# Kernel tuning notes

Hardware: AMD Instinct MI355X
Metric: run time of the kernel (lower is better)

## Reference

```python
import jax, jax.numpy as jnp
import numpy as np

DIM = 768
H = 12          # num_heads
HD = DIM // H   # head_dim = 64
WS = 128        # window_size
SHIFT = 64      # shift_size
NPATCH = 128    # num_patches for relative bias
MLP = 3072
EPS = 1e-5


def _layernorm(x, w, b):
    m = jnp.mean(x, axis=-1, keepdims=True)
    v = jnp.mean(jnp.square(x - m), axis=-1, keepdims=True)
    return (x - m) * jax.lax.rsqrt(v + EPS) * w + b


def _window_attention(xw, mw, qkv_w, qkv_b, proj_w, proj_b, rel_bias):
    # xw: [Bw, ws, C] windows, mw: [Bw, ws] bool valid-key mask
    Bw, N, C = xw.shape
    qkv = (xw @ qkv_w + qkv_b).reshape(Bw, N, 3, H, HD)
    qkv = jnp.transpose(qkv, (2, 0, 3, 1, 4))  # [3, Bw, H, N, hd]
    q, k, v = qkv[0], qkv[1], qkv[2]
    attn = jnp.einsum('bhqd,bhkd->bhqk', q, k) * (HD ** -0.5)
    # relative position bias: table [2*NPATCH-1, H] gathered by index [N, N]
    coords = jnp.arange(N)
    rel_idx = coords[None, :] - coords[:, None] + (NPATCH - 1)  # [N, N]
    bias = jnp.transpose(rel_bias[rel_idx], (2, 0, 1))  # [H, N, N]
    attn = attn + bias[None]
    neg = jnp.finfo(attn.dtype).min
    attn = jnp.where(mw[:, None, None, :], attn, neg)  # mask invalid keys
    attn = jax.nn.softmax(attn, axis=-1)
    attn = jnp.nan_to_num(attn, nan=0.0)
    out = jnp.einsum('bhqk,bhkd->bqhd', attn, v).reshape(Bw, N, C)
    return out @ proj_w + proj_b


def reference(x, norm1_w, norm1_b, qkv_w, qkv_b, proj_w, proj_b, rel_bias,
              ls1, norm2_w, norm2_b, fc1_w, fc1_b, fc2_w, fc2_b, ls2):
    B, N, C = x.shape
    # ---- attention branch: norm1 -> shifted-window attention ----
    h = _layernorm(x, norm1_w, norm1_b)
    pad = (-N) % WS
    hp = jnp.pad(h, ((0, 0), (0, pad), (0, 0)))  # zero-pad sequence
    Npad = N + pad
    valid = jnp.broadcast_to(jnp.arange(Npad) < N, (B, Npad))
    if SHIFT > 0:
        hp = jnp.roll(hp, -SHIFT, axis=1)
        valid = jnp.roll(valid, -SHIFT, axis=1)
    nw = Npad // WS
    xw = hp.reshape(B * nw, WS, C)
    mw = valid.reshape(B * nw, WS)
    aw = _window_attention(xw, mw, qkv_w, qkv_b, proj_w, proj_b, rel_bias)
    a = aw.reshape(B, Npad, C)
    if SHIFT > 0:
        a = jnp.roll(a, SHIFT, axis=1)
    a = a[:, :N, :]
    x = x + a * ls1  # LayerScale, DropPath is identity
    # ---- MLP branch ----
    h2 = _layernorm(x, norm2_w, norm2_b)
    m = jax.nn.gelu(h2 @ fc1_w + fc1_b, approximate=False) @ fc2_w + fc2_b
    return x + m * ls2


def setup_inputs() -> dict:
    key = jax.random.key(0)
    ks = jax.random.split(key, 8)
    B, N = 16, 2000
    s = 0.02
    return {
        'x': jax.random.normal(ks[0], (B, N, DIM), jnp.float32),
        'norm1_w': jnp.ones((DIM,), jnp.float32),
        'norm1_b': jnp.zeros((DIM,), jnp.float32),
        'qkv_w': s * jax.random.normal(ks[1], (DIM, 3 * DIM), jnp.float32),
        'qkv_b': jnp.zeros((3 * DIM,), jnp.float32),
        'proj_w': s * jax.random.normal(ks[2], (DIM, DIM), jnp.float32),
        'proj_b': jnp.zeros((DIM,), jnp.float32),
        'rel_bias': s * jax.random.normal(ks[3], (2 * NPATCH - 1, H), jnp.float32),
        'ls1': 1e-5 * jnp.ones((DIM,), jnp.float32),
        'norm2_w': jnp.ones((DIM,), jnp.float32),
        'norm2_b': jnp.zeros((DIM,), jnp.float32),
        'fc1_w': s * jax.random.normal(ks[4], (DIM, MLP), jnp.float32),
        'fc1_b': jnp.zeros((MLP,), jnp.float32),
        'fc2_w': s * jax.random.normal(ks[5], (MLP, DIM), jnp.float32),
        'fc2_b': jnp.zeros((DIM,), jnp.float32),
        'ls2': 1e-5 * jnp.ones((DIM,), jnp.float32),
    }
```

## Files before the change

kernel.cpp:

```cpp
#include <hip/hip_runtime.h>
#include <hip/hip_bf16.h>

typedef unsigned short u16;
typedef unsigned char u8;
typedef __attribute__((ext_vector_type(8))) short bh8;
typedef __attribute__((ext_vector_type(4))) float fx4;
typedef __attribute__((ext_vector_type(4))) int i32x4;
typedef __attribute__((ext_vector_type(8))) int i32x8;

__device__ __forceinline__ u16 f2bf(float f) {
  union { float f; unsigned u; } v; v.f = f;
  unsigned r = v.u + 0x7FFFu + ((v.u >> 16) & 1u);
  return (u16)(r >> 16);
}

__device__ __forceinline__ u8 f2fp8(float x) {
  union { float f; unsigned u; } v; v.f = x;
  const unsigned sign = (v.u >> 24) & 0x80u;
  v.u &= 0x7FFFFFFFu;
  if (v.f >= 464.0f) return (u8)(sign | 0x7Eu);
  if (v.f < 0.015625f) {
    int q = (int)rintf(v.f * 512.0f);
    return (u8)(sign | (unsigned)q);
  }
  unsigned u2 = v.u + 0x7FFFFu + ((v.u >> 20) & 1u);
  unsigned e2 = (u2 >> 23) - 127u + 7u;
  unsigned mant = (u2 >> 20) & 7u;
  return (u8)(sign | (e2 << 3) | mant);
}

__device__ __forceinline__ void cvt2_fp8(float a, float b, u8& x, u8& y) {
#if __has_builtin(__builtin_amdgcn_cvt_pk_fp8_f32)
  int r = __builtin_amdgcn_cvt_pk_fp8_f32(a, b, 0, false);
  x = (u8)(r & 0xff);
  y = (u8)((r >> 8) & 0xff);
#else
  x = f2fp8(a);
  y = f2fp8(b);
#endif
}

__device__ __forceinline__ float fp8_manual(u8 b) {
  unsigned s = b >> 7, e = (b >> 3) & 15, m = b & 7;
  float v;
  if (e == 0) {
    v = m * 0.001953125f;
  } else {
    union { unsigned u; float f; } t;
    t.u = ((e + 120u) << 23) | (m << 20);
    v = t.f;
  }
  return s ? -v : v;
}

__device__ __forceinline__ void fp8dec4(unsigned w, float* o) {
#if __has_builtin(__builtin_amdgcn_cvt_f32_fp8)
  o[0] = __builtin_amdgcn_cvt_f32_fp8((int)w, 0);
  o[1] = __builtin_amdgcn_cvt_f32_fp8((int)w, 1);
  o[2] = __builtin_amdgcn_cvt_f32_fp8((int)w, 2);
  o[3] = __builtin_amdgcn_cvt_f32_fp8((int)w, 3);
#else
  o[0] = fp8_manual((u8)(w & 0xffu));
  o[1] = fp8_manual((u8)((w >> 8) & 0xffu));
  o[2] = fp8_manual((u8)((w >> 16) & 0xffu));
  o[3] = fp8_manual((u8)((w >> 24) & 0xffu));
#endif
}

__device__ __forceinline__ void gload_lds16(const void* g, void* l) {
  __builtin_amdgcn_global_load_lds(
      (const __attribute__((address_space(1))) void*)g,
      (__attribute__((address_space(3))) void*)l, 16, 0, 0);
}

__device__ __forceinline__ i32x8 rd32(const char* p0, const char* p1) {
  i32x4 lo = *(const i32x4*)p0;
  i32x4 hi = *(const i32x4*)p1;
  return __builtin_shufflevector(lo, hi, 0, 1, 2, 3, 4, 5, 6, 7);
}

__global__ __launch_bounds__(256) void transp_cvt(
    const float* __restrict__ W, u8* __restrict__ Wt, int K, int N) {
  __shared__ float tile[32][33];
  const int k0 = blockIdx.x * 32, n0 = blockIdx.y * 32;
  const int tx = threadIdx.x & 31, ty = threadIdx.x >> 5;
#pragma unroll
  for (int i = 0; i < 4; ++i)
    tile[ty + i * 8][tx] = W[(size_t)(k0 + ty + i * 8) * N + n0 + tx];
  __syncthreads();
#pragma unroll
  for (int i = 0; i < 4; ++i)
    Wt[(size_t)(n0 + ty + i * 8) * K + k0 + tx] = f2fp8(tile[tx][ty + i * 8] * 32.0f);
}

__device__ __forceinline__ float blockSum(float v, float* sh) {
#pragma unroll
  for (int m = 32; m; m >>= 1) v += __shfl_xor(v, m);
  if ((threadIdx.x & 63) == 0) sh[threadIdx.x >> 6] = v;
  __syncthreads();
  return sh[0] + sh[1] + sh[2] + sh[3];
}

__global__ __launch_bounds__(256) void ln1_k(
    const float* __restrict__ x, const float* __restrict__ w,
    const float* __restrict__ b, u8* __restrict__ hw) {
  __shared__ float sh1[4], sh2[4];
  const int row = blockIdx.x;
  const int bI = row >> 11, i = row & 2047;
  const int j = (i + 64) & 2047;
  const int tid = threadIdx.x;
  u8* dst = hw + (size_t)row * 768;
  if (j >= 2000) {
    dst[tid] = 0; dst[tid + 256] = 0; dst[tid + 512] = 0;
    return;
  }
  const float* xr = x + ((size_t)bI * 2000 + j) * 768;
  float v0 = xr[tid], v1 = xr[tid + 256], v2 = xr[tid + 512];
  float mean = blockSum(v0 + v1 + v2, sh1) * (1.0f / 768.0f);
  float d0 = v0 - mean, d1 = v1 - mean, d2 = v2 - mean;
  float var = blockSum(d0 * d0 + d1 * d1 + d2 * d2, sh2) * (1.0f / 768.0f);
  float rs = rsqrtf(var + 1e-5f);
  u8 x0, x1, x2, xd;
  cvt2_fp8((d0 * rs * w[tid] + b[tid]) * 4.0f,
           (d1 * rs * w[tid + 256] + b[tid + 256]) * 4.0f, x0, x1);
  cvt2_fp8((d2 * rs * w[tid + 512] + b[tid + 512]) * 4.0f, 0.0f, x2, xd);
  dst[tid] = x0; dst[tid + 256] = x1; dst[tid + 512] = x2;
}

__global__ __launch_bounds__(256) void ln2_k(
    const float* __restrict__ src, const float* __restrict__ w,
    const float* __restrict__ b, u8* __restrict__ dsth) {
  __shared__ float sh1[4], sh2[4];
  const int row = blockIdx.x;
  const int tid = threadIdx.x;
  const float* xr = src + (size_t)row * 768;
  u8* dst = dsth + (size_t)row * 768;
  float v0 = xr[tid], v1 = xr[tid + 256], v2 = xr[tid + 512];
  float mean = blockSum(v0 + v1 + v2, sh1) * (1.0f / 768.0f);
  float d0 = v0 - mean, d1 = v1 - mean, d2 = v2 - mean;
  float var = blockSum(d0 * d0 + d1 * d1 + d2 * d2, sh2) * (1.0f / 768.0f);
  float rs = rsqrtf(var + 1e-5f);
  u8 x0, x1, x2, xd;
  cvt2_fp8((d0 * rs * w[tid] + b[tid]) * 4.0f,
           (d1 * rs * w[tid + 256] + b[tid + 256]) * 4.0f, x0, x1);
  cvt2_fp8((d2 * rs * w[tid + 512] + b[tid + 512]) * 4.0f, 0.0f, x2, xd);
  dst[tid] = x0; dst[tid + 256] = x1; dst[tid + 512] = x2;
}

enum { EQKV = 0, EPROJ = 1, EFC1 = 2, EFC2 = 3 };

template <int EPI>
__global__ __launch_bounds__(256, 3) void gemm128f8(
    const u8* __restrict__ A, const u8* __restrict__ Bt,
    const float* __restrict__ bias, const float* __restrict__ lsv,
    const float* __restrict__ resid, float* __restrict__ outf,
    u8* __restrict__ outb,
    int gn, int N, int K, int mValid) {
  __shared__ u8 LDSBUF[32768];
  u8* As = LDSBUF;
  u8* Bs = LDSBUF + 16384;
  const int tid = threadIdx.x;
  const int lane = tid & 63, wid = tid >> 6;
  const int wr = wid >> 1, wc = wid & 1;

  const int nwg = gridDim.x, bid = blockIdx.x;
  const int q = nwg >> 3, r = nwg & 7;
  const int xcd = bid & 7, idx = bid >> 3;
  const int wg = (xcd < r ? xcd * (q + 1) : r * (q + 1) + (xcd - r) * q) + idx;
  const int mt = wg / gn, nt = wg % gn;
  const int m0 = mt * 128, n0 = nt * 128;
  const int NT = K >> 7;

  fx4 acc[4][4];
#pragma unroll
  for (int i = 0; i < 4; ++i)
#pragma unroll
    for (int j = 0; j < 4; ++j) acc[i][j] = fx4{0.f, 0.f, 0.f, 0.f};

  const int rsel = lane & 15, kgrp = lane >> 4;
  const int colb = kgrp * 32;
  const int xorc = (rsel & 7) << 4;

  const int rl = tid >> 3;
  const int kc16 = ((tid & 7) ^ (rl & 7)) * 16;
  const u8* aRow = A + (size_t)(m0 + rl) * K + kc16;
  const u8* bRow = Bt + (size_t)(n0 + rl) * K + kc16;

  for (int t = 0; t < NT; ++t) {
    const int k0 = t << 7;
#pragma unroll
    for (int i = 0; i < 4; ++i) {
      gload_lds16(aRow + (size_t)k0 + (size_t)(i * 32) * K,
                  (char*)As + i * 4096 + wid * 1024);
      gload_lds16(bRow + (size_t)k0 + (size_t)(i * 32) * K,
                  (char*)Bs + i * 4096 + wid * 1024);
    }
    __syncthreads();
    i32x8 af[4];
#pragma unroll
    for (int mi = 0; mi < 4; ++mi) {
      const char* ab = (const char*)As + (wr * 64 + mi * 16 + rsel) * 128;
      af[mi] = rd32(ab + (colb ^ xorc), ab + ((colb + 16) ^ xorc));
    }
#pragma unroll
    for (int ni = 0; ni < 4; ++ni) {
      const char* bb = (const char*)Bs + (wc * 64 + ni * 16 + rsel) * 128;
      i32x8 bfr = rd32(bb + (colb ^ xorc), bb + ((colb + 16) ^ xorc));
#pragma unroll
      for (int mi = 0; mi < 4; ++mi)
        acc[mi][ni] = __builtin_amdgcn_mfma_scale_f32_16x16x128_f8f6f4(
            af[mi], bfr, acc[mi][ni], 0, 0, 0, 125, 0, 122);
    }
    __syncthreads();
  }

  const int cc = lane & 15;
  const int rq = (lane >> 4) * 4;

  if (EPI == EQKV || EPI == EFC1) {
    u8* Ls = LDSBUF;
#pragma unroll
    for (int ni = 0; ni < 4; ++ni) {
      const int col = wc * 64 + ni * 16 + cc;
      const float bv = bias[n0 + col];
#pragma unroll
      for (int mi = 0; mi < 4; ++mi) {
#pragma unroll
        for (int jp = 0; jp < 2; ++jp) {
          float va = acc[mi][ni][jp * 2] + bv;
          float vb = acc[mi][ni][jp * 2 + 1] + bv;
          if (EPI == EFC1) {
            va = va / (1.0f + __expf(-1.702f * va));
            vb = vb / (1.0f + __expf(-1.702f * vb));
          }
          u8 xa, xb;
          cvt2_fp8(va * 4.0f, vb * 4.0f, xa, xb);
          const int row = wr * 64 + mi * 16 + rq + jp * 2;
          const int s = (row & 12) << 2;
          Ls[row * 128 + (col ^ s)] = xa;
          Ls[(row + 1) * 128 + (col ^ s)] = xb;
        }
      }
    }
    __syncthreads();
#pragma unroll
    for (int i = 0; i < 4; ++i) {
      const int row = i * 32 + (tid >> 3);
      const int s = (row & 12) << 2;
      i32x4 v = *(const i32x4*)(Ls + row * 128 + (((tid & 7) * 16) ^ s));
      *(i32x4*)(outb + (size_t)(m0 + row) * N + n0 + (tid & 7) * 16) = v;
    }
  } else {
    float* Lf = (float*)LDSBUF;
#pragma unroll
    for (int p = 0; p < 2; ++p) {
      if (p) __syncthreads();
      if (wc == p) {
#pragma unroll
        for (int ni = 0; ni < 4; ++ni) {
          const int gc = n0 + p * 64 + ni * 16 + cc;
          const float bv = bias[gc], ls = lsv[gc];
#pragma unroll
          for (int mi = 0; mi < 4; ++mi)
#pragma unroll
            for (int j = 0; j < 4; ++j) {
              const int row = wr * 64 + mi * 16 + rq + j;
              const int s = (row & 12) << 2;
              Lf[row * 64 + ((ni * 16 + cc) ^ s)] = (acc[mi][ni][j] + bv) * ls;
            }
        }
      }
      __syncthreads();
#pragma unroll
      for (int i = 0; i < 8; ++i) {
        const int row = i * 16 + (tid >> 4);
        const int gr = m0 + row;
        const int s = (row & 12) << 2;
        fx4 sv = *(const fx4*)(Lf + row * 64 + (((tid & 15) * 4) ^ s));
        if (EPI == EFC2) {
          if (gr < mValid) {
            float* po = outf + (size_t)gr * 768 + n0 + p * 64 + (tid & 15) * 4;
            fx4 cur = *(const fx4*)po;
            *(fx4*)po = fx4{cur[0] + sv[0], cur[1] + sv[1], cur[2] + sv[2], cur[3] + sv[3]};
          }
        } else {
          const int bI = gr >> 11, ip = gr & 2047;
          const int jj = (ip + 64) & 2047;
          if (jj < 2000) {
            const size_t o = ((size_t)bI * 2000 + jj) * 768 + n0 + p * 64 + (tid & 15) * 4;
            fx4 rv = *(const fx4*)(resid + o);
            *(fx4*)(outf + o) = fx4{rv[0] + sv[0], rv[1] + sv[1], rv[2] + sv[2], rv[3] + sv[3]};
          }
        }
      }
    }
  }
}

struct AttnLds {
  union {
    struct { u16 Qs[128][72]; u16 Ks[128][72]; } qk;
    u16 Ps[128][136];
  } u;
  u16 Vt[64][136];
  float biasv[256];
};

__global__ __launch_bounds__(256, 2) void attn_k(
    const u8* __restrict__ qkv8, const float* __restrict__ rel_bias,
    u8* __restrict__ aout) {
  __shared__ AttnLds L;
  const int blk = blockIdx.x;
  const int w = blk / 12, h = blk - w * 12;
  const int wi = w & 15;
  const int tid = threadIdx.x;
  const int lane = tid & 63, wid = tid >> 6;

  if (tid < 255) L.biasv[tid] = rel_bias[tid * 12 + h];

  const size_t rowbase = (size_t)w * 128;
#pragma unroll
  for (int i = 0; i < 4; ++i) {
    const int idx = tid + i * 256;
    const int r = idx >> 3, seg = idx & 7;
    const u8* src = qkv8 + (rowbase + r) * 2304 + h * 64 + seg * 8;
    unsigned qlo = *(const unsigned*)(src);
    unsigned qhi = *(const unsigned*)(src + 4);
    unsigned klo = *(const unsigned*)(src + 768);
    unsigned khi = *(const unsigned*)(src + 772);
    unsigned vlo = *(const unsigned*)(src + 1536);
    unsigned vhi = *(const unsigned*)(src + 1540);
    float qf[8], kf[8], vf[8];
    fp8dec4(qlo, qf); fp8dec4(qhi, qf + 4);
    fp8dec4(klo, kf); fp8dec4(khi, kf + 4);
    fp8dec4(vlo, vf); fp8dec4(vhi, vf + 4);
    bh8 qv, kv;
    u16 va[8];
#pragma unroll
    for (int e = 0; e < 8; ++e) {
      qv[e] = (short)f2bf(qf[e] * 0.25f);
      kv[e] = (short)f2bf(kf[e] * 0.25f);
      va[e] = f2bf(vf[e] * 0.25f);
    }
    *(bh8*)&L.u.qk.Qs[r][seg * 8] = qv;
    *(bh8*)&L.u.qk.Ks[r][seg * 8] = kv;
#pragma unroll
    for (int e = 0; e < 8; ++e) L.Vt[seg * 8 + e][r] = va[e];
  }
  __syncthreads();

  const int R0 = wid * 32;
  const int rsel = lane & 15, kgrp = lane >> 4;
  fx4 s[2][8];
#pragma unroll
  for (int mi = 0; mi < 2; ++mi)
#pragma unroll
    for (int ni = 0; ni < 8; ++ni) s[mi][ni] = fx4{0.f, 0.f, 0.f, 0.f};

#pragma unroll
  for (int ks = 0; ks < 2; ++ks) {
    bh8 aq[2], bk[8];
#pragma unroll
    for (int mi = 0; mi < 2; ++mi)
      aq[mi] = *(const bh8*)&L.u.qk.Qs[R0 + mi * 16 + rsel][ks * 32 + kgrp * 8];
#pragma unroll
    for (int ni = 0; ni < 8; ++ni)
      bk[ni] = *(const bh8*)&L.u.qk.Ks[ni * 16 + rsel][ks * 32 + kgrp * 8];
#pragma unroll
    for (int mi = 0; mi < 2; ++mi)
#pragma unroll
      for (int ni = 0; ni < 8; ++ni)
        s[mi][ni] = __builtin_amdgcn_mfma_f32_16x16x32_bf16(aq[mi], bk[ni], s[mi][ni], 0, 0, 0);
  }

#pragma unroll
  for (int mi = 0; mi < 2; ++mi) {
#pragma unroll
    for (int j = 0; j < 4; ++j) {
      const int r = R0 + mi * 16 + kgrp * 4 + j;
      float vals[8];
      float mx = -1e30f;
#pragma unroll
      for (int ni = 0; ni < 8; ++ni) {
        const int c = ni * 16 + rsel;
        const int ic = wi * 128 + c;
        const bool valid = ((ic + 64) & 2047) < 2000;
        const float v = valid ? (s[mi][ni][j] * 0.125f + L.biasv[c - r + 127]) : -1e30f;
        vals[ni] = v;
        mx = fmaxf(mx, v);
      }
#pragma unroll
      for (int mm = 8; mm; mm >>= 1) mx = fmaxf(mx, __shfl_xor(mx, mm));
      float sum = 0.f;
#pragma unroll
      for (int ni = 0; ni < 8; ++ni) { float p = __expf(vals[ni] - mx); vals[ni] = p; sum += p; }
#pragma unroll
      for (int mm = 8; mm; mm >>= 1) sum += __shfl_xor(sum, mm);
      const float inv = 1.0f / sum;
#pragma unroll
      for (int ni = 0; ni < 8; ++ni) s[mi][ni][j] = vals[ni] * inv;
    }
  }
  __syncthreads();

#pragma unroll
  for (int mi = 0; mi < 2; ++mi)
#pragma unroll
    for (int ni = 0; ni < 8; ++ni)
#pragma unroll
      for (int j = 0; j < 4; ++j)
        L.u.Ps[R0 + mi * 16 + kgrp * 4 + j][ni * 16 + rsel] = f2bf(s[mi][ni][j]);
  __syncthreads();

  fx4 o[2][4];
#pragma unroll
  for (int mi = 0; mi < 2; ++mi)
#pragma unroll
    for (int ni = 0; ni < 4; ++ni) o[mi][ni] = fx4{0.f, 0.f, 0.f, 0.f};
#pragma unroll
  for (int ks = 0; ks < 4; ++ks) {
    bh8 ap[2], bv[4];
#pragma unroll
    for (int mi = 0; mi < 2; ++mi)
      ap[mi] = *(const bh8*)&L.u.Ps[R0 + mi * 16 + rsel][ks * 32 + kgrp * 8];
#pragma unroll
    for (int ni = 0; ni < 4; ++ni)
      bv[ni] = *(const bh8*)&L.Vt[ni * 16 + rsel][ks * 32 + kgrp * 8];
#pragma unroll
    for (int mi = 0; mi < 2; ++mi)
#pragma unroll
      for (int ni = 0; ni < 4; ++ni)
        o[mi][ni] = __builtin_amdgcn_mfma_f32_16x16x32_bf16(ap[mi], bv[ni], o[mi][ni], 0, 0, 0);
  }

#pragma unroll
  for (int mi = 0; mi < 2; ++mi)
#pragma unroll
    for (int ni = 0; ni < 4; ++ni)
#pragma unroll
      for (int jp = 0; jp < 2; ++jp) {
        u8 xa, xb;
        cvt2_fp8(o[mi][ni][jp * 2] * 4.0f, o[mi][ni][jp * 2 + 1] * 4.0f, xa, xb);
        const size_t r0 = rowbase + R0 + mi * 16 + kgrp * 4 + jp * 2;
        aout[r0 * 768 + h * 64 + ni * 16 + rsel] = xa;
        aout[(r0 + 1) * 768 + h * 64 + ni * 16 + rsel] = xb;
      }
}

extern "C" void kernel_launch(void* const* d_in, const int* in_sizes, int n_in,
                              void* d_out, int out_size, void* d_ws, size_t ws_size,
                              hipStream_t stream) {
  (void)in_sizes; (void)n_in; (void)out_size; (void)ws_size;
  const float* x        = (const float*)d_in[0];
  const float* n1w      = (const float*)d_in[1];
  const float* n1b      = (const float*)d_in[2];
  const float* qkv_w    = (const float*)d_in[3];
  const float* qkv_b    = (const float*)d_in[4];
  const float* proj_w   = (const float*)d_in[5];
  const float* proj_b   = (const float*)d_in[6];
  const float* rel_bias = (const float*)d_in[7];
  const float* ls1      = (const float*)d_in[8];
  const float* n2w      = (const float*)d_in[9];
  const float* n2b      = (const float*)d_in[10];
  const float* fc1_w    = (const float*)d_in[11];
  const float* fc1_b    = (const float*)d_in[12];
  const float* fc2_w    = (const float*)d_in[13];
  const float* fc2_b    = (const float*)d_in[14];
  const float* ls2      = (const float*)d_in[15];
  float* out = (float*)d_out;

  char* ws = (char*)d_ws;
  u8*  WtQ   = (u8*)(ws);
  u8*  WtP   = (u8*)(ws + 3538944);
  u8*  WtF1  = (u8*)(ws + 4718592);
  u8*  WtF2  = (u8*)(ws + 9437184);
  u8*  bufB8 = (u8*)(ws + 14155776);
  u8*  bufA8 = (u8*)(ws + 14155776 + 50331648);

  dim3 t256(256);
  transp_cvt<<<dim3(24, 72), t256, 0, stream>>>(qkv_w, WtQ, 768, 2304);
  transp_cvt<<<dim3(24, 24), t256, 0, stream>>>(proj_w, WtP, 768, 768);
  transp_cvt<<<dim3(24, 96), t256, 0, stream>>>(fc1_w, WtF1, 768, 3072);
  transp_cvt<<<dim3(96, 24), t256, 0, stream>>>(fc2_w, WtF2, 3072, 768);

  ln1_k<<<32768, t256, 0, stream>>>(x, n1w, n1b, bufB8);
  gemm128f8<EQKV><<<dim3(256 * 18), t256, 0, stream>>>(
      bufB8, WtQ, qkv_b, nullptr, nullptr, nullptr, bufA8, 18, 2304, 768, 32768);
  attn_k<<<3072, t256, 0, stream>>>(bufA8, rel_bias, bufB8);
  gemm128f8<EPROJ><<<dim3(256 * 6), t256, 0, stream>>>(
      bufB8, WtP, proj_b, ls1, x, out, nullptr, 6, 768, 768, 32768);
  ln2_k<<<32000, t256, 0, stream>>>(out, n2w, n2b, bufB8);
  gemm128f8<EFC1><<<dim3(250 * 24), t256, 0, stream>>>(
      bufB8, WtF1, fc1_b, nullptr, nullptr, nullptr, bufA8, 24, 3072, 768, 32000);
  gemm128f8<EFC2><<<dim3(250 * 6), t256, 0, stream>>>(
      bufA8, WtF2, fc2_b, ls2, nullptr, out, nullptr, 6, 768, 3072, 32000);
}
```

Before: 502.6 us.

## Use 8 waves per block in FP8 GEMM with 64x32 per-wave tiles

Doubles the GEMM workgroup from 256 to 512 threads. Each wave now computes a 64x32 sub-tile instead of 64x64, so accumulator registers are halved and per-thread global-to-LDS loads drop from 8 to 4. The epilogues are remapped to the new wave layout. The aim is more waves in flight to hide latency, at the cost of more LDS fragment reads per MFMA, since each A fragment is reused only twice.

```diff
diff --git a/kernel.cpp b/kernel.cpp
--- a/kernel.cpp
+++ b/kernel.cpp
@@ -150,7 +150,7 @@
 enum { EQKV = 0, EPROJ = 1, EFC1 = 2, EFC2 = 3 };
 
 template <int EPI>
-__global__ __launch_bounds__(256, 3) void gemm128f8(
+__global__ __launch_bounds__(512, 4) void gemm128f8(
     const u8* __restrict__ A, const u8* __restrict__ Bt,
     const float* __restrict__ bias, const float* __restrict__ lsv,
     const float* __restrict__ resid, float* __restrict__ outf,
@@ -161,7 +161,7 @@
   u8* Bs = LDSBUF + 16384;
   const int tid = threadIdx.x;
   const int lane = tid & 63, wid = tid >> 6;
-  const int wr = wid >> 1, wc = wid & 1;
+  const int wr = wid >> 2, wc = wid & 3;
 
   const int nwg = gridDim.x, bid = blockIdx.x;
   const int q = nwg >> 3, r = nwg & 7;
@@ -171,11 +171,11 @@
   const int m0 = mt * 128, n0 = nt * 128;
   const int NT = K >> 7;
 
-  fx4 acc[4][4];
+  fx4 acc[4][2];
 #pragma unroll
   for (int i = 0; i < 4; ++i)
 #pragma unroll
-    for (int j = 0; j < 4; ++j) acc[i][j] = fx4{0.f, 0.f, 0.f, 0.f};
+    for (int j = 0; j < 2; ++j) acc[i][j] = fx4{0.f, 0.f, 0.f, 0.f};
 
   const int rsel = lane & 15, kgrp = lane >> 4;
   const int colb = kgrp * 32;
@@ -188,28 +188,25 @@
 
   for (int t = 0; t < NT; ++t) {
     const int k0 = t << 7;
-#pragma unroll
-    for (int i = 0; i < 4; ++i) {
-      gload_lds16(aRow + (size_t)k0 + (size_t)(i * 32) * K,
-                  (char*)As + i * 4096 + wid * 1024);
-      gload_lds16(bRow + (size_t)k0 + (size_t)(i * 32) * K,
-                  (char*)Bs + i * 4096 + wid * 1024);
-    }
+    gload_lds16(aRow + (size_t)k0, (char*)As + wid * 1024);
+    gload_lds16(aRow + (size_t)k0 + (size_t)64 * K, (char*)As + 8192 + wid * 1024);
+    gload_lds16(bRow + (size_t)k0, (char*)Bs + wid * 1024);
+    gload_lds16(bRow + (size_t)k0 + (size_t)64 * K, (char*)Bs + 8192 + wid * 1024);
     __syncthreads();
-    i32x8 af[4];
+    i32x8 bq[2];
+#pragma unroll
+    for (int n2 = 0; n2 < 2; ++n2) {
+      const char* bb = (const char*)Bs + (wc * 32 + n2 * 16 + rsel) * 128;
+      bq[n2] = rd32(bb + (colb ^ xorc), bb + ((colb + 16) ^ xorc));
+    }
 #pragma unroll
     for (int mi = 0; mi < 4; ++mi) {
       const char* ab = (const char*)As + (wr * 64 + mi * 16 + rsel) * 128;
-      af[mi] = rd32(ab + (colb ^ xorc), ab + ((colb + 16) ^ xorc));
-    }
-#pragma unroll
-    for (int ni = 0; ni < 4; ++ni) {
-      const char* bb = (const char*)Bs + (wc * 64 + ni * 16 + rsel) * 128;
-      i32x8 bfr = rd32(bb + (colb ^ xorc), bb + ((colb + 16) ^ xorc));
-#pragma unroll
-      for (int mi = 0; mi < 4; ++mi)
-        acc[mi][ni] = __builtin_amdgcn_mfma_scale_f32_16x16x128_f8f6f4(
-            af[mi], bfr, acc[mi][ni], 0, 0, 0, 125, 0, 122);
+      i32x8 af = rd32(ab + (colb ^ xorc), ab + ((colb + 16) ^ xorc));
+#pragma unroll
+      for (int n2 = 0; n2 < 2; ++n2)
+        acc[mi][n2] = __builtin_amdgcn_mfma_scale_f32_16x16x128_f8f6f4(
+            af, bq[n2], acc[mi][n2], 0, 0, 0, 125, 0, 122);
     }
     __syncthreads();
   }
@@ -220,15 +217,15 @@
   if (EPI == EQKV || EPI == EFC1) {
     u8* Ls = LDSBUF;
 #pragma unroll
-    for (int ni = 0; ni < 4; ++ni) {
-      const int col = wc * 64 + ni * 16 + cc;
+    for (int n2 = 0; n2 < 2; ++n2) {
+      const int col = wc * 32 + n2 * 16 + cc;
       const float bv = bias[n0 + col];
 #pragma unroll
       for (int mi = 0; mi < 4; ++mi) {
 #pragma unroll
         for (int jp = 0; jp < 2; ++jp) {
-          float va = acc[mi][ni][jp * 2] + bv;
-          float vb = acc[mi][ni][jp * 2 + 1] + bv;
+          float va = acc[mi][n2][jp * 2] + bv;
+          float vb = acc[mi][n2][jp * 2 + 1] + bv;
           if (EPI == EFC1) {
             va = va / (1.0f + __expf(-1.702f * va));
             vb = vb / (1.0f + __expf(-1.702f * vb));
@@ -244,8 +241,8 @@
     }
     __syncthreads();
 #pragma unroll
-    for (int i = 0; i < 4; ++i) {
-      const int row = i * 32 + (tid >> 3);
+    for (int i = 0; i < 2; ++i) {
+      const int row = i * 64 + (tid >> 3);
       const int s = (row & 12) << 2;
       i32x4 v = *(const i32x4*)(Ls + row * 128 + (((tid & 7) * 16) ^ s));
       *(i32x4*)(outb + (size_t)(m0 + row) * N + n0 + (tid & 7) * 16) = v;
@@ -255,10 +252,11 @@
 #pragma unroll
     for (int p = 0; p < 2; ++p) {
       if (p) __syncthreads();
-      if (wc == p) {
-#pragma unroll
-        for (int ni = 0; ni < 4; ++ni) {
-          const int gc = n0 + p * 64 + ni * 16 + cc;
+      if ((wc >> 1) == p) {
+#pragma unroll
+        for (int n2 = 0; n2 < 2; ++n2) {
+          const int lcol = (wc & 1) * 32 + n2 * 16 + cc;
+          const int gc = n0 + p * 64 + lcol;
           const float bv = bias[gc], ls = lsv[gc];
 #pragma unroll
           for (int mi = 0; mi < 4; ++mi)
@@ -266,14 +264,14 @@
             for (int j = 0; j < 4; ++j) {
               const int row = wr * 64 + mi * 16 + rq + j;
               const int s = (row & 12) << 2;
-              Lf[row * 64 + ((ni * 16 + cc) ^ s)] = (acc[mi][ni][j] + bv) * ls;
+              Lf[row * 64 + (lcol ^ s)] = (acc[mi][n2][j] + bv) * ls;
             }
         }
       }
       __syncthreads();
 #pragma unroll
-      for (int i = 0; i < 8; ++i) {
-        const int row = i * 16 + (tid >> 4);
+      for (int i = 0; i < 4; ++i) {
+        const int row = i * 32 + (tid >> 4);
         const int gr = m0 + row;
         const int s = (row & 12) << 2;
         fx4 sv = *(const fx4*)(Lf + row * 64 + (((tid & 15) * 4) ^ s));
@@ -477,21 +475,21 @@
   u8*  bufB8 = (u8*)(ws + 14155776);
   u8*  bufA8 = (u8*)(ws + 14155776 + 50331648);
 
-  dim3 t256(256);
+  dim3 t256(256), t512(512);
   transp_cvt<<<dim3(24, 72), t256, 0, stream>>>(qkv_w, WtQ, 768, 2304);
   transp_cvt<<<dim3(24, 24), t256, 0, stream>>>(proj_w, WtP, 768, 768);
   transp_cvt<<<dim3(24, 96), t256, 0, stream>>>(fc1_w, WtF1, 768, 3072);
   transp_cvt<<<dim3(96, 24), t256, 0, stream>>>(fc2_w, WtF2, 3072, 768);
 
   ln1_k<<<32768, t256, 0, stream>>>(x, n1w, n1b, bufB8);
-  gemm128f8<EQKV><<<dim3(256 * 18), t256, 0, stream>>>(
+  gemm128f8<EQKV><<<dim3(256 * 18), t512, 0, stream>>>(
       bufB8, WtQ, qkv_b, nullptr, nullptr, nullptr, bufA8, 18, 2304, 768, 32768);
   attn_k<<<3072, t256, 0, stream>>>(bufA8, rel_bias, bufB8);
-  gemm128f8<EPROJ><<<dim3(256 * 6), t256, 0, stream>>>(
+  gemm128f8<EPROJ><<<dim3(256 * 6), t512, 0, stream>>>(
       bufB8, WtP, proj_b, ls1, x, out, nullptr, 6, 768, 768, 32768);
   ln2_k<<<32000, t256, 0, stream>>>(out, n2w, n2b, bufB8);
-  gemm128f8<EFC1><<<dim3(250 * 24), t256, 0, stream>>>(
+  gemm128f8<EFC1><<<dim3(250 * 24), t512, 0, stream>>>(
       bufB8, WtF1, fc1_b, nullptr, nullptr, nullptr, bufA8, 24, 3072, 768, 32000);
-  gemm128f8<EFC2><<<dim3(250 * 6), t256, 0, stream>>>(
+  gemm128f8<EFC2><<<dim3(250 * 6), t512, 0, stream>>>(
       bufA8, WtF2, fc2_b, ls2, nullptr, out, nullptr, 6, 768, 3072, 32000);
 }
```

Measured after the change: 512.0 us. Within noise of the previous version (+1.9%).
